# Kernel tuning notes

Hardware: AMD Instinct MI355X
Metric: run time of the kernel (lower is better)

Reference implementation:

```python
import jax, jax.numpy as jnp
import numpy as np
from jax import lax

VOCAB = 12000
EMB = 512
RNN = 512
FEATS = 4096
SEQ_LEN = 15


def setup_inputs() -> dict:
    key = jax.random.key(0)
    ks = jax.random.split(key, 10)
    B = 1024
    s = 0.05
    return {
        "img_features": jax.random.normal(ks[0], (B, FEATS), jnp.float32),
        "W_feats": jax.random.normal(ks[1], (EMB, FEATS), jnp.float32) * s,
        "b_feats": jax.random.normal(ks[2], (EMB,), jnp.float32) * s,
        "W_ih": jax.random.normal(ks[3], (4 * RNN, EMB), jnp.float32) * s,
        "W_hh": jax.random.normal(ks[4], (4 * RNN, RNN), jnp.float32) * s,
        "b_ih": jax.random.normal(ks[5], (4 * RNN,), jnp.float32) * s,
        "b_hh": jax.random.normal(ks[6], (4 * RNN,), jnp.float32) * s,
        "emb": jax.random.normal(ks[7], (VOCAB, EMB), jnp.float32) * s,
        "W_out": jax.random.normal(ks[8], (VOCAB - 2, RNN), jnp.float32) * s,
        "b_out": jax.random.normal(ks[9], (VOCAB - 2,), jnp.float32) * s,
    }


def reference(img_features, W_feats, b_feats, W_ih, W_hh, b_ih, b_hh, emb, W_out, b_out):
    B = img_features.shape[0]

    def lstm_cell(x, h, c):
        # torch.nn.LSTMCell: gates ordered i, f, g, o
        gates = x @ W_ih.T + b_ih + h @ W_hh.T + b_hh
        i, f, g, o = jnp.split(gates, 4, axis=1)
        c_new = jax.nn.sigmoid(f) * c + jax.nn.sigmoid(i) * jnp.tanh(g)
        h_new = jax.nn.sigmoid(o) * jnp.tanh(c_new)
        return h_new, c_new

    # image feature embedding + ReLU, then prime the LSTM with it
    img_vec = jax.nn.relu(img_features @ W_feats.T + b_feats)  # [B, 512]
    h = jnp.zeros((B, RNN), img_features.dtype)
    c = jnp.zeros((B, RNN), img_features.dtype)
    h, c = lstm_cell(img_vec, h, c)

    def step(carry, _):
        h, c, words = carry
        x = emb[words]                     # [B, 512] embedding lookup
        h, c = lstm_cell(x, h, c)
        logits = h @ W_out.T + b_out       # [B, VOCAB-2]
        idx = jnp.argmax(logits, axis=1).astype(jnp.int32)
        return (h, c, idx + 2), idx

    words0 = jnp.ones((B,), jnp.int32)  # START token = 1
    _, seq = lax.scan(step, (h, c, words0), None, length=SEQ_LEN)
    return seq.T  # [B, SEQ_LEN] greedy-decoded token ids
```

## Files before the change

kernel.cpp:

```cpp
#include <hip/hip_runtime.h>
#include <stdint.h>

#define BATCH  1024
#define SEQLEN 15
#define NGATE  2048
#define NVOCAB 11998
#define FEATS  4096

typedef __attribute__((ext_vector_type(8)))  short  s8v;
typedef __attribute__((ext_vector_type(16))) float  f32x16;
typedef __attribute__((ext_vector_type(8)))  unsigned short us8;

__device__ __forceinline__ unsigned short f2bf(float f) {
    unsigned u = __float_as_uint(f);
    u += 0x7FFFu + ((u >> 16) & 1u);
    return (unsigned short)(u >> 16);
}
__device__ __forceinline__ float bf2f(unsigned short h) {
    return __uint_as_float(((unsigned)h) << 16);
}
struct bfpair { unsigned short hi, lo; };
__device__ __forceinline__ bfpair split2v(float v) {
    bfpair r;
    r.hi = f2bf(v);
    r.lo = f2bf(v - bf2f(r.hi));
    return r;
}
__device__ __forceinline__ void split8(const float* __restrict__ s, us8& vh, us8& vl) {
    #pragma unroll
    for (int e = 0; e < 8; ++e) {
        bfpair q = split2v(s[e]);
        vh[e] = q.hi; vl[e] = q.lo;
    }
}

__device__ __forceinline__ void async_cp16(const void* g, void* l) {
    __builtin_amdgcn_global_load_lds(
        (const __attribute__((address_space(1))) unsigned int*)g,
        (__attribute__((address_space(3))) unsigned int*)l, 16, 0, 0);
}

__global__ void prep_wcat_blk(const float* __restrict__ W_ih, const float* __restrict__ W_hh,
                              const float* __restrict__ b_ih, const float* __restrict__ b_hh,
                              unsigned short* __restrict__ hi, unsigned short* __restrict__ lo,
                              float* __restrict__ bsum) {
    int idx = blockIdx.x * 256 + threadIdx.x;
    int kc = idx >> 11, row = idx & 2047;
    int k = kc << 3;
    const float* src = (k < 512) ? (W_ih + (size_t)row * 512 + k)
                                 : (W_hh + (size_t)row * 512 + (k - 512));
    us8 vh, vl; split8(src, vh, vl);
    *(us8*)(hi + (size_t)idx * 8) = vh;
    *(us8*)(lo + (size_t)idx * 8) = vl;
    if (idx < NGATE) bsum[idx] = b_ih[idx] + b_hh[idx];
}

__global__ void prep_blk(const float* __restrict__ src,
                         unsigned short* __restrict__ hi, unsigned short* __restrict__ lo,
                         int R, int K) {
    int row = blockIdx.x * 256 + threadIdx.x;
    if (row >= R) return;
    int kc = blockIdx.y;
    us8 vh, vl; split8(src + (size_t)row * K + (kc << 3), vh, vl);
    size_t o = ((size_t)kc * R + row) * 8;
    *(us8*)(hi + o) = vh;
    *(us8*)(lo + o) = vl;
}

__device__ __forceinline__ void mfma_blk_store(
    const unsigned short* __restrict__ Ahi, const unsigned short* __restrict__ Alo, int aRows,
    const unsigned short* __restrict__ Bhi, const unsigned short* __restrict__ Blo, int bRows,
    float* __restrict__ C, int ldc,
    int K, size_t akstride, size_t bkstride, size_t czstride)
{
    __shared__ short smem[4 * 4 * 128 * 8];
    short* sAhi = smem;
    short* sAlo = smem + 4 * 128 * 8;
    short* sBhi = smem + 2 * 4 * 128 * 8;
    short* sBlo = smem + 3 * 4 * 128 * 8;

    const int kz = blockIdx.z;
    Ahi += (size_t)kz * akstride;  Alo += (size_t)kz * akstride;
    Bhi += (size_t)kz * bkstride;  Blo += (size_t)kz * bkstride;
    C   += (size_t)kz * czstride;

    const int tid  = threadIdx.x;
    const int lane = tid & 63, wave = tid >> 6;
    const int wr = (wave & 1) * 64, wc = (wave >> 1) * 64;
    const int col = lane & 31, kh = lane >> 5;
    const int bm = blockIdx.y * 128, bn = blockIdx.x * 128;

    f32x16 acc[2][2] = {};

    for (int k0 = 0; k0 < K; k0 += 32) {
        const int kc0 = k0 >> 3;
        __syncthreads();
        #pragma unroll
        for (int p = 0; p < 2; ++p) {
            int s    = p * 4 + wave;
            int kc_l = s >> 1, rh = s & 1;
            int rl   = rh * 64 + lane;
            int lo_  = (kc_l * 128 + rh * 64) * 8;
            size_t ga = ((size_t)(kc0 + kc_l) * aRows + (bm + rl)) * 8;
            async_cp16(Ahi + ga, sAhi + lo_);
            async_cp16(Alo + ga, sAlo + lo_);
            int brow = bn + rl; if (brow > bRows - 1) brow = bRows - 1;
            size_t gb = ((size_t)(kc0 + kc_l) * bRows + brow) * 8;
            async_cp16(Bhi + gb, sBhi + lo_);
            async_cp16(Blo + gb, sBlo + lo_);
        }
        __syncthreads();

        #pragma unroll
        for (int st = 0; st < 2; ++st) {
            int off = (2 * st + kh) * 128 * 8;
            s8v ah0 = *(const s8v*)(sAhi + off + (wr + col) * 8);
            s8v ah1 = *(const s8v*)(sAhi + off + (wr + 32 + col) * 8);
            s8v al0 = *(const s8v*)(sAlo + off + (wr + col) * 8);
            s8v al1 = *(const s8v*)(sAlo + off + (wr + 32 + col) * 8);
            s8v bh0 = *(const s8v*)(sBhi + off + (wc + col) * 8);
            s8v bh1 = *(const s8v*)(sBhi + off + (wc + 32 + col) * 8);
            s8v bl0 = *(const s8v*)(sBlo + off + (wc + col) * 8);
            s8v bl1 = *(const s8v*)(sBlo + off + (wc + 32 + col) * 8);
            acc[0][0] = __builtin_amdgcn_mfma_f32_32x32x16_bf16(ah0, bh0, acc[0][0], 0, 0, 0);
            acc[0][1] = __builtin_amdgcn_mfma_f32_32x32x16_bf16(ah0, bh1, acc[0][1], 0, 0, 0);
            acc[1][0] = __builtin_amdgcn_mfma_f32_32x32x16_bf16(ah1, bh0, acc[1][0], 0, 0, 0);
            acc[1][1] = __builtin_amdgcn_mfma_f32_32x32x16_bf16(ah1, bh1, acc[1][1], 0, 0, 0);
            acc[0][0] = __builtin_amdgcn_mfma_f32_32x32x16_bf16(ah0, bl0, acc[0][0], 0, 0, 0);
            acc[0][1] = __builtin_amdgcn_mfma_f32_32x32x16_bf16(ah0, bl1, acc[0][1], 0, 0, 0);
            acc[1][0] = __builtin_amdgcn_mfma_f32_32x32x16_bf16(ah1, bl0, acc[1][0], 0, 0, 0);
            acc[1][1] = __builtin_amdgcn_mfma_f32_32x32x16_bf16(ah1, bl1, acc[1][1], 0, 0, 0);
            acc[0][0] = __builtin_amdgcn_mfma_f32_32x32x16_bf16(al0, bh0, acc[0][0], 0, 0, 0);
            acc[0][1] = __builtin_amdgcn_mfma_f32_32x32x16_bf16(al0, bh1, acc[0][1], 0, 0, 0);
            acc[1][0] = __builtin_amdgcn_mfma_f32_32x32x16_bf16(al1, bh0, acc[1][0], 0, 0, 0);
            acc[1][1] = __builtin_amdgcn_mfma_f32_32x32x16_bf16(al1, bh1, acc[1][1], 0, 0, 0);
        }
    }

    #pragma unroll
    for (int i = 0; i < 2; ++i)
        #pragma unroll
        for (int rg = 0; rg < 4; ++rg)
            #pragma unroll
            for (int rr = 0; rr < 4; ++rr) {
                int reg = rg * 4 + rr;
                int m = bm + wr + i * 32 + rr + rg * 8 + kh * 4;
                #pragma unroll
                for (int j = 0; j < 2; ++j) {
                    int n = bn + wc + j * 32 + col;
                    if (n < bRows) C[(size_t)m * ldc + n] = acc[i][j][reg];
                }
            }
}

__global__ __launch_bounds__(256) void k_gemm_gates(
    const unsigned short* Ahi, const unsigned short* Alo,
    const unsigned short* Bhi, const unsigned short* Blo,
    float* C, size_t aks, size_t bks, size_t czs) {
    mfma_blk_store(Ahi, Alo, 1024, Bhi, Blo, NGATE, C, NGATE, 512, aks, bks, czs);
}
__global__ __launch_bounds__(256) void k_gemm_feats(
    const unsigned short* Ahi, const unsigned short* Alo,
    const unsigned short* Bhi, const unsigned short* Blo,
    float* C) {
    mfma_blk_store(Ahi, Alo, 1024, Bhi, Blo, 512, C, 512, 512,
                   (size_t)64 * 1024 * 8, (size_t)64 * 512 * 8, (size_t)1024 * 512);
}

__global__ __launch_bounds__(128, 2) void k_logits_argmax(
    const unsigned short* __restrict__ h_hi, const unsigned short* __restrict__ h_lo,
    const unsigned short* __restrict__ wout_hi, const unsigned short* __restrict__ wout_lo,
    const float* __restrict__ bias, unsigned long long* __restrict__ packed) {
    __shared__ short smem[4 * 4 * 128 * 8];
    short* sAhi = smem;
    short* sAlo = smem + 4096;
    short* sBhi = smem + 8192;
    short* sBlo = smem + 12288;

    const int tid = threadIdx.x;
    const int lane = tid & 63, wave = tid >> 6;
    const int wr = wave * 64;
    const int col = lane & 31, kh = lane >> 5;
    const int bm = blockIdx.y * 128, bn = blockIdx.x * 128;
    const int aRows = 1024, bRows = NVOCAB;

    f32x16 acc[2][4] = {};

    for (int k0 = 0; k0 < 512; k0 += 32) {
        const int kc0 = k0 >> 3;
        __syncthreads();
        #pragma unroll
        for (int p = 0; p < 16; ++p) {
            int s = p * 2 + wave;
            int arr = s >> 3, rem = s & 7;
            int kc_l = rem >> 1, rh = rem & 1;
            int rl = rh * 64 + lane;
            int lo_ = (kc_l * 128 + rh * 64) * 8;
            if (arr < 2) {
                size_t ga = ((size_t)(kc0 + kc_l) * aRows + (bm + rl)) * 8;
                async_cp16((arr == 0 ? h_hi : h_lo) + ga, (arr == 0 ? sAhi : sAlo) + lo_);
            } else {
                int brow = bn + rl; if (brow > bRows - 1) brow = bRows - 1;
                size_t gb = ((size_t)(kc0 + kc_l) * bRows + brow) * 8;
                async_cp16((arr == 2 ? wout_hi : wout_lo) + gb, (arr == 2 ? sBhi : sBlo) + lo_);
            }
        }
        __syncthreads();

        #pragma unroll
        for (int st = 0; st < 2; ++st) {
            int off = (2 * st + kh) * 128 * 8;
            s8v ah0 = *(const s8v*)(sAhi + off + (wr + col) * 8);
            s8v ah1 = *(const s8v*)(sAhi + off + (wr + 32 + col) * 8);
            s8v al0 = *(const s8v*)(sAlo + off + (wr + col) * 8);
            s8v al1 = *(const s8v*)(sAlo + off + (wr + 32 + col) * 8);
            #pragma unroll
            for (int j = 0; j < 4; ++j) {
                s8v bh = *(const s8v*)(sBhi + off + (j * 32 + col) * 8);
                s8v bl = *(const s8v*)(sBlo + off + (j * 32 + col) * 8);
                acc[0][j] = __builtin_amdgcn_mfma_f32_32x32x16_bf16(ah0, bh, acc[0][j], 0, 0, 0);
                acc[1][j] = __builtin_amdgcn_mfma_f32_32x32x16_bf16(ah1, bh, acc[1][j], 0, 0, 0);
                acc[0][j] = __builtin_amdgcn_mfma_f32_32x32x16_bf16(ah0, bl, acc[0][j], 0, 0, 0);
                acc[1][j] = __builtin_amdgcn_mfma_f32_32x32x16_bf16(ah1, bl, acc[1][j], 0, 0, 0);
                acc[0][j] = __builtin_amdgcn_mfma_f32_32x32x16_bf16(al0, bh, acc[0][j], 0, 0, 0);
                acc[1][j] = __builtin_amdgcn_mfma_f32_32x32x16_bf16(al1, bh, acc[1][j], 0, 0, 0);
            }
        }
    }

    #pragma unroll
    for (int i = 0; i < 2; ++i)
        #pragma unroll
        for (int rg = 0; rg < 4; ++rg)
            #pragma unroll
            for (int rr = 0; rr < 4; ++rr) {
                int reg = rg * 4 + rr;
                int m = bm + wr + i * 32 + rr + rg * 8 + kh * 4;
                unsigned long long best = 0ull;
                #pragma unroll
                for (int j = 0; j < 4; ++j) {
                    int n = bn + j * 32 + col;
                    if (n < bRows) {
                        float v = acc[i][j][reg] + bias[n];
                        unsigned int u   = __float_as_uint(v);
                        unsigned int key = (u & 0x80000000u) ? ~u : (u | 0x80000000u);
                        unsigned long long pk =
                            ((unsigned long long)key << 32) |
                            (unsigned long long)(0xFFFFFFFFu - (unsigned)n);
                        best = (pk > best) ? pk : best;
                    }
                }
                #pragma unroll
                for (int sdist = 1; sdist < 32; sdist <<= 1) {
                    unsigned long long o = __shfl_xor(best, sdist, 64);
                    best = (o > best) ? o : best;
                }
                if (col == 0) atomicMax(&packed[m], best);
            }
}

__global__ void feats_reduce8(const float* __restrict__ part, const float* __restrict__ bias,
                              unsigned short* __restrict__ hi, unsigned short* __restrict__ lo) {
    int idx = blockIdx.x * 256 + threadIdx.x;
    int b = idx >> 6, kc = idx & 63;
    int n = kc << 3;
    float v[8];
    #pragma unroll
    for (int e = 0; e < 8; ++e) v[e] = bias[n + e];
    #pragma unroll
    for (int z = 0; z < 8; ++z) {
        const float* s = part + (size_t)z * 1024 * 512 + (size_t)b * 512 + n;
        #pragma unroll
        for (int e = 0; e < 8; ++e) v[e] += s[e];
    }
    us8 vh, vl;
    #pragma unroll
    for (int e = 0; e < 8; ++e) {
        bfpair q = split2v(fmaxf(v[e], 0.f));
        vh[e] = q.hi; vl[e] = q.lo;
    }
    size_t o = ((size_t)kc * 1024 + b) * 8;
    *(us8*)(hi + o) = vh;
    *(us8*)(lo + o) = vl;
}

template<bool PRIME>
__global__ void lstm_pw_blk(const float* __restrict__ g0, const float* __restrict__ g1,
                            const float* __restrict__ bsum, float* __restrict__ cbuf,
                            unsigned short* __restrict__ xh_hi, unsigned short* __restrict__ xh_lo,
                            unsigned long long* __restrict__ packed,
                            int* __restrict__ out, int t) {
    int idx = blockIdx.x * 256 + threadIdx.x;
    int b = idx >> 6, j8 = idx & 63;
    int j = j8 << 3;
    const float* g = g0 + (size_t)b * NGATE;
    float v[4][8];
    #pragma unroll
    for (int gt = 0; gt < 4; ++gt) {
        const float* s = g + gt * 512 + j;
        const float* bs = bsum + gt * 512 + j;
        #pragma unroll
        for (int e = 0; e < 8; ++e) v[gt][e] = s[e] + bs[e];
    }
    if (!PRIME) {
        const float* h2 = g1 + (size_t)b * NGATE;
        #pragma unroll
        for (int gt = 0; gt < 4; ++gt) {
            const float* s = h2 + gt * 512 + j;
            #pragma unroll
            for (int e = 0; e < 8; ++e) v[gt][e] += s[e];
        }
    }
    float* cb = cbuf + (size_t)b * 512 + j;
    us8 vh, vl;
    #pragma unroll
    for (int e = 0; e < 8; ++e) {
        float si = 1.f / (1.f + expf(-v[0][e]));
        float sf = 1.f / (1.f + expf(-v[1][e]));
        float tg = tanhf(v[2][e]);
        float so = 1.f / (1.f + expf(-v[3][e]));
        float cn = PRIME ? (si * tg) : (sf * cb[e] + si * tg);
        cb[e] = cn;
        bfpair q = split2v(so * tanhf(cn));
        vh[e] = q.hi; vl[e] = q.lo;
    }
    size_t o = ((size_t)(64 + j8) * 1024 + b) * 8;
    *(us8*)(xh_hi + o) = vh;
    *(us8*)(xh_lo + o) = vl;
    if (j8 == 0) {
        if (!PRIME && t > 0) {
            unsigned long long p = packed[b];
            out[b * SEQLEN + (t - 1)] = (int)(0xFFFFFFFFu - (unsigned)(p & 0xFFFFFFFFull));
        }
        packed[b] = 0ull;
    }
}

template<int FIRST>
__global__ void gather_blk(const float* __restrict__ emb,
                           const unsigned long long* __restrict__ packed,
                           unsigned short* __restrict__ xh_hi, unsigned short* __restrict__ xh_lo) {
    int idx = blockIdx.x * 256 + threadIdx.x;
    int b = idx >> 6, kc = idx & 63;
    int word = 1;
    if (!FIRST) {
        unsigned long long p = packed[b];
        word = (int)(0xFFFFFFFFu - (unsigned)(p & 0xFFFFFFFFull)) + 2;
    }
    us8 vh, vl; split8(emb + (size_t)word * 512 + (kc << 3), vh, vl);
    size_t o = ((size_t)kc * 1024 + b) * 8;
    *(us8*)(xh_hi + o) = vh;
    *(us8*)(xh_lo + o) = vl;
}

__global__ void final_out(const unsigned long long* __restrict__ packed, int* __restrict__ out) {
    int b = blockIdx.x * 256 + threadIdx.x;
    if (b < BATCH) {
        unsigned long long p = packed[b];
        out[b * SEQLEN + (SEQLEN - 1)] = (int)(0xFFFFFFFFu - (unsigned)(p & 0xFFFFFFFFull));
    }
}

extern "C" void kernel_launch(void* const* d_in, const int* in_sizes, int n_in,
                              void* d_out, int out_size, void* d_ws, size_t ws_size,
                              hipStream_t stream) {
    const float* img     = (const float*)d_in[0];
    const float* W_feats = (const float*)d_in[1];
    const float* b_feats = (const float*)d_in[2];
    const float* W_ih    = (const float*)d_in[3];
    const float* W_hh    = (const float*)d_in[4];
    const float* b_ih    = (const float*)d_in[5];
    const float* b_hh    = (const float*)d_in[6];
    const float* emb     = (const float*)d_in[7];
    const float* W_out   = (const float*)d_in[8];
    const float* b_out   = (const float*)d_in[9];
    int* out = (int*)d_out;

    const size_t WCAT_H = (size_t)128 * 2048 * 8;
    const size_t WOUT_H = (size_t)64 * NVOCAB * 8;
    const size_t XH_H   = (size_t)128 * 1024 * 8;
    const size_t IMGV_H = (size_t)64 * 1024 * 8;

    char* p = (char*)d_ws;
    unsigned short* wcat_hi = (unsigned short*)p;  p += WCAT_H * 2;
    unsigned short* wcat_lo = (unsigned short*)p;  p += WCAT_H * 2;
    unsigned short* wout_hi = (unsigned short*)p;  p += WOUT_H * 2;
    unsigned short* wout_lo = (unsigned short*)p;  p += WOUT_H * 2;
    unsigned short* xh_hi   = (unsigned short*)p;  p += XH_H * 2;
    unsigned short* xh_lo   = (unsigned short*)p;  p += XH_H * 2;
    unsigned short* imgv_hi = (unsigned short*)p;  p += IMGV_H * 2;
    unsigned short* imgv_lo = (unsigned short*)p;  p += IMGV_H * 2;
    float* cbuf             = (float*)p;           p += (size_t)1024 * 512 * 4;
    float* bsum             = (float*)p;           p += (size_t)NGATE * 4;
    unsigned long long* packed = (unsigned long long*)p;  p += (size_t)1024 * 8;
    float* gates0           = (float*)p;           p += (size_t)1024 * NGATE * 4;
    float* gates1           = (float*)p;           p += (size_t)1024 * NGATE * 4;
    unsigned short* imgb_hi = wout_hi;
    unsigned short* imgb_lo = imgb_hi + (size_t)512 * 1024 * 8;
    unsigned short* wfb_hi  = imgb_lo + (size_t)512 * 1024 * 8;
    unsigned short* wfb_lo  = wfb_hi  + (size_t)512 * 512 * 8;
    float* partials = gates0;

    prep_wcat_blk<<<1024, 256, 0, stream>>>(W_ih, W_hh, b_ih, b_hh, wcat_hi, wcat_lo, bsum);
    prep_blk<<<dim3(4, 512), 256, 0, stream>>>(img,     imgb_hi, imgb_lo, 1024, FEATS);
    prep_blk<<<dim3(2, 512), 256, 0, stream>>>(W_feats, wfb_hi,  wfb_lo,  512,  FEATS);

    k_gemm_feats<<<dim3(4, 8, 8), 256, 0, stream>>>(imgb_hi, imgb_lo, wfb_hi, wfb_lo, partials);
    feats_reduce8<<<256, 256, 0, stream>>>(partials, b_feats, imgv_hi, imgv_lo);

    prep_blk<<<dim3(47, 64), 256, 0, stream>>>(W_out, wout_hi, wout_lo, NVOCAB, 512);

    k_gemm_gates<<<dim3(16, 8, 1), 256, 0, stream>>>(imgv_hi, imgv_lo, wcat_hi, wcat_lo,
                                                     gates0, 0, 0, 0);
    lstm_pw_blk<true><<<256, 256, 0, stream>>>(gates0, nullptr, bsum, cbuf,
                                               xh_hi, xh_lo, packed, out, 0);

    for (int t = 0; t < SEQLEN; ++t) {
        if (t == 0) gather_blk<1><<<256, 256, 0, stream>>>(emb, packed, xh_hi, xh_lo);
        else        gather_blk<0><<<256, 256, 0, stream>>>(emb, packed, xh_hi, xh_lo);
        k_gemm_gates<<<dim3(16, 8, 2), 256, 0, stream>>>(
            xh_hi, xh_lo, wcat_hi, wcat_lo, gates0,
            (size_t)64 * 1024 * 8, (size_t)64 * 2048 * 8, (size_t)1024 * NGATE);
        lstm_pw_blk<false><<<256, 256, 0, stream>>>(gates0, gates1, bsum, cbuf,
                                                    xh_hi, xh_lo, packed, out, t);
        k_logits_argmax<<<dim3(94, 8), 128, 0, stream>>>(
            xh_hi + (size_t)64 * 1024 * 8, xh_lo + (size_t)64 * 1024 * 8,
            wout_hi, wout_lo, b_out, packed);
    }
    final_out<<<4, 256, 0, stream>>>(packed, out);
}
```

Measured before the change: 1.764 ms.

## Shrink logits tile to 64x64 single-wave blocks with XCD-aware block mapping

The logits+argmax GEMM moves from 128x128 tiles with two waves per block to 64x64 tiles handled by one wave, launched as 3072 blocks. Blocks are mapped so that each XCD (block id mod 8) owns a contiguous range of vocab columns, which should keep that XCD's slice of W_out in its local L2. The aim is more parallel blocks and better cache locality for the weight matrix. The cost is less reuse per tile, so more global and LDS traffic per flop, and more atomicMax calls on the packed argmax.

Measured after the change: 2.443 ms. 1.39x slower.

```diff
diff --git a/kernel.cpp b/kernel.cpp
--- a/kernel.cpp
+++ b/kernel.cpp
@@ -167,64 +167,70 @@
                    (size_t)64 * 1024 * 8, (size_t)64 * 512 * 8, (size_t)1024 * 512);
 }
 
-__global__ __launch_bounds__(128, 2) void k_logits_argmax(
+__global__ __launch_bounds__(64, 2) void k_logits_argmax(
     const unsigned short* __restrict__ h_hi, const unsigned short* __restrict__ h_lo,
     const unsigned short* __restrict__ wout_hi, const unsigned short* __restrict__ wout_lo,
     const float* __restrict__ bias, unsigned long long* __restrict__ packed) {
-    __shared__ short smem[4 * 4 * 128 * 8];
+    __shared__ short smem[4 * 2048];
     short* sAhi = smem;
-    short* sAlo = smem + 4096;
-    short* sBhi = smem + 8192;
-    short* sBlo = smem + 12288;
-
-    const int tid = threadIdx.x;
-    const int lane = tid & 63, wave = tid >> 6;
-    const int wr = wave * 64;
+    short* sAlo = smem + 2048;
+    short* sBhi = smem + 4096;
+    short* sBlo = smem + 6144;
+
+    const int lane = threadIdx.x;
     const int col = lane & 31, kh = lane >> 5;
-    const int bm = blockIdx.y * 128, bn = blockIdx.x * 128;
+
+    const int id = blockIdx.x;
+    const int xcd = id & 7, slot = id >> 3;
+    const int bn_t = xcd * 24 + (slot % 24);
+    const int bm_t = slot / 24;
+    const int bm = bm_t * 64, bn = bn_t * 64;
     const int aRows = 1024, bRows = NVOCAB;
 
-    f32x16 acc[2][4] = {};
+    f32x16 acc[2][2] = {};
 
     for (int k0 = 0; k0 < 512; k0 += 32) {
         const int kc0 = k0 >> 3;
         __syncthreads();
         #pragma unroll
-        for (int p = 0; p < 16; ++p) {
-            int s = p * 2 + wave;
-            int arr = s >> 3, rem = s & 7;
-            int kc_l = rem >> 1, rh = rem & 1;
-            int rl = rh * 64 + lane;
-            int lo_ = (kc_l * 128 + rh * 64) * 8;
+        for (int s = 0; s < 16; ++s) {
+            int arr = s >> 2, kc_l = s & 3;
             if (arr < 2) {
-                size_t ga = ((size_t)(kc0 + kc_l) * aRows + (bm + rl)) * 8;
-                async_cp16((arr == 0 ? h_hi : h_lo) + ga, (arr == 0 ? sAhi : sAlo) + lo_);
+                size_t ga = ((size_t)(kc0 + kc_l) * aRows + (bm + lane)) * 8;
+                async_cp16((arr == 0 ? h_hi : h_lo) + ga,
+                           (arr == 0 ? sAhi : sAlo) + kc_l * 512);
             } else {
-                int brow = bn + rl; if (brow > bRows - 1) brow = bRows - 1;
+                int brow = bn + lane; if (brow > bRows - 1) brow = bRows - 1;
                 size_t gb = ((size_t)(kc0 + kc_l) * bRows + brow) * 8;
-                async_cp16((arr == 2 ? wout_hi : wout_lo) + gb, (arr == 2 ? sBhi : sBlo) + lo_);
+                async_cp16((arr == 2 ? wout_hi : wout_lo) + gb,
+                           (arr == 2 ? sBhi : sBlo) + kc_l * 512);
             }
         }
         __syncthreads();
 
         #pragma unroll
         for (int st = 0; st < 2; ++st) {
-            int off = (2 * st + kh) * 128 * 8;
-            s8v ah0 = *(const s8v*)(sAhi + off + (wr + col) * 8);
-            s8v ah1 = *(const s8v*)(sAhi + off + (wr + 32 + col) * 8);
-            s8v al0 = *(const s8v*)(sAlo + off + (wr + col) * 8);
-            s8v al1 = *(const s8v*)(sAlo + off + (wr + 32 + col) * 8);
-            #pragma unroll
-            for (int j = 0; j < 4; ++j) {
-                s8v bh = *(const s8v*)(sBhi + off + (j * 32 + col) * 8);
-                s8v bl = *(const s8v*)(sBlo + off + (j * 32 + col) * 8);
-                acc[0][j] = __builtin_amdgcn_mfma_f32_32x32x16_bf16(ah0, bh, acc[0][j], 0, 0, 0);
-                acc[1][j] = __builtin_amdgcn_mfma_f32_32x32x16_bf16(ah1, bh, acc[1][j], 0, 0, 0);
-                acc[0][j] = __builtin_amdgcn_mfma_f32_32x32x16_bf16(ah0, bl, acc[0][j], 0, 0, 0);
-                acc[1][j] = __builtin_amdgcn_mfma_f32_32x32x16_bf16(ah1, bl, acc[1][j], 0, 0, 0);
-                acc[0][j] = __builtin_amdgcn_mfma_f32_32x32x16_bf16(al0, bh, acc[0][j], 0, 0, 0);
-                acc[1][j] = __builtin_amdgcn_mfma_f32_32x32x16_bf16(al1, bh, acc[1][j], 0, 0, 0);
-            }
+            int off = (2 * st + kh) * 512;
+            s8v ah0 = *(const s8v*)(sAhi + off + col * 8);
+            s8v ah1 = *(const s8v*)(sAhi + off + (32 + col) * 8);
+            s8v al0 = *(const s8v*)(sAlo + off + col * 8);
+            s8v al1 = *(const s8v*)(sAlo + off + (32 + col) * 8);
+            s8v bh0 = *(const s8v*)(sBhi + off + col * 8);
+            s8v bh1 = *(const s8v*)(sBhi + off + (32 + col) * 8);
+            s8v bl0 = *(const s8v*)(sBlo + off + col * 8);
+            s8v bl1 = *(const s8v*)(sBlo + off + (32 + col) * 8);
+            acc[0][0] = __builtin_amdgcn_mfma_f32_32x32x16_bf16(ah0, bh0, acc[0][0], 0, 0, 0);
+            acc[0][1] = __builtin_amdgcn_mfma_f32_32x32x16_bf16(ah0, bh1, acc[0][1], 0, 0, 0);
+            acc[1][0] = __builtin_amdgcn_mfma_f32_32x32x16_bf16(ah1, bh0, acc[1][0], 0, 0, 0);
+            acc[1][1] = __builtin_amdgcn_mfma_f32_32x32x16_bf16(ah1, bh1, acc[1][1], 0, 0, 0);
+            acc[0][0] = __builtin_amdgcn_mfma_f32_32x32x16_bf16(ah0, bl0, acc[0][0], 0, 0, 0);
+            acc[0][1] = __builtin_amdgcn_mfma_f32_32x32x16_bf16(ah0, bl1, acc[0][1], 0, 0, 0);
+            acc[1][0] = __builtin_amdgcn_mfma_f32_32x32x16_bf16(ah1, bl0, acc[1][0], 0, 0, 0);
+            acc[1][1] = __builtin_amdgcn_mfma_f32_32x32x16_bf16(ah1, bl1, acc[1][1], 0, 0, 0);
+            acc[0][0] = __builtin_amdgcn_mfma_f32_32x32x16_bf16(al0, bh0, acc[0][0], 0, 0, 0);
+            acc[0][1] = __builtin_amdgcn_mfma_f32_32x32x16_bf16(al0, bh1, acc[0][1], 0, 0, 0);
+            acc[1][0] = __builtin_amdgcn_mfma_f32_32x32x16_bf16(al1, bh0, acc[1][0], 0, 0, 0);
+            acc[1][1] = __builtin_amdgcn_mfma_f32_32x32x16_bf16(al1, bh1, acc[1][1], 0, 0, 0);
         }
     }
 
@@ -235,10 +241,10 @@
             #pragma unroll
             for (int rr = 0; rr < 4; ++rr) {
                 int reg = rg * 4 + rr;
-                int m = bm + wr + i * 32 + rr + rg * 8 + kh * 4;
+                int m = bm + i * 32 + rr + rg * 8 + kh * 4;
                 unsigned long long best = 0ull;
                 #pragma unroll
-                for (int j = 0; j < 4; ++j) {
+                for (int j = 0; j < 2; ++j) {
                     int n = bn + j * 32 + col;
                     if (n < bRows) {
                         float v = acc[i][j][reg] + bias[n];
@@ -423,7 +429,7 @@
             (size_t)64 * 1024 * 8, (size_t)64 * 2048 * 8, (size_t)1024 * NGATE);
         lstm_pw_blk<false><<<256, 256, 0, stream>>>(gates0, gates1, bsum, cbuf,
                                                     xh_hi, xh_lo, packed, out, t);
-        k_logits_argmax<<<dim3(94, 8), 128, 0, stream>>>(
+        k_logits_argmax<<<3072, 64, 0, stream>>>(
             xh_hi + (size_t)64 * 1024 * 8, xh_lo + (size_t)64 * 1024 * 8,
             wout_hi, wout_lo, b_out, packed);
     }
```
